# Performance work log

Hardware: AMD Instinct MI355X
Metric: run time of the kernel (lower is better)

The kernel has to match this reference:

```python
import jax, jax.numpy as jnp
import numpy as np

B, T, E, D, V, L, A = 32, 800, 512, 1024, 5000, 149, 512
SOS, EOS = 1, 2


def setup_inputs() -> dict:
    key = jax.random.key(0)
    ks = jax.random.split(key, 20)
    s = 0.02
    inp = {
        'hpad': jax.random.normal(ks[0], (B, T, E), dtype=jnp.float32),
        'hlen': jax.random.randint(ks[1], (B,), T // 2, T + 1),
        'ys': jax.random.randint(ks[2], (B, L), 3, V),
        # embedding + output projection
        'embed': jax.random.normal(ks[3], (V, D), dtype=jnp.float32) * s,
        'W_out': jax.random.normal(ks[4], (V, D), dtype=jnp.float32) * s,
        'b_out': jnp.zeros((V,), dtype=jnp.float32),
        # additive attention params
        'W_enc': jax.random.normal(ks[5], (E, A), dtype=jnp.float32) * s,
        'W_dec': jax.random.normal(ks[6], (D, A), dtype=jnp.float32) * s,
        'v_att': jax.random.normal(ks[7], (A,), dtype=jnp.float32) * s,
        # LSTMCell layer 0: input = [ey; att_c] of size D+E
        'W_ih0': jax.random.normal(ks[8], (4 * D, D + E), dtype=jnp.float32) * s,
        'b_ih0': jnp.zeros((4 * D,), dtype=jnp.float32),
        'W_hh0': jax.random.normal(ks[9], (4 * D, D), dtype=jnp.float32) * s,
        'b_hh0': jnp.zeros((4 * D,), dtype=jnp.float32),
        # LSTMCell layer 1: input = z0 of size D
        'W_ih1': jax.random.normal(ks[10], (4 * D, D), dtype=jnp.float32) * s,
        'b_ih1': jnp.zeros((4 * D,), dtype=jnp.float32),
        'W_hh1': jax.random.normal(ks[11], (4 * D, D), dtype=jnp.float32) * s,
        'b_hh1': jnp.zeros((4 * D,), dtype=jnp.float32),
    }
    return inp


def _lstm_cell(x, h, c, W_ih, b_ih, W_hh, b_hh):
    # torch.nn.LSTMCell gate order: i, f, g, o
    g = x @ W_ih.T + b_ih + h @ W_hh.T + b_hh
    i, f, gg, o = jnp.split(g, 4, axis=-1)
    c2 = jax.nn.sigmoid(f) * c + jax.nn.sigmoid(i) * jnp.tanh(gg)
    h2 = jax.nn.sigmoid(o) * jnp.tanh(c2)
    return h2, c2


def reference(hpad, hlen, ys, embed, W_out, b_out, W_enc, W_dec, v_att,
              W_ih0, b_ih0, W_hh0, b_hh0, W_ih1, b_ih1, W_hh1, b_hh1):
    mask = jnp.arange(T)[None, :] < hlen[:, None]          # [B,T]
    hpad = hpad * mask[..., None]                          # mask_by_length
    ys_in = jnp.concatenate([jnp.full((B, 1), SOS, ys.dtype), ys], axis=1)   # [B,L+1]
    ys_out = jnp.concatenate([ys, jnp.full((B, 1), EOS, ys.dtype)], axis=1)  # [B,L+1]
    eys = embed[ys_in]                                     # [B,L+1,D]
    pe = jnp.einsum('bte,ea->bta', hpad, W_enc)            # precomputed enc proj

    def step(carry, ey):
        z0, c0, z1, c1 = carry
        # additive attention: e = v^T tanh(W_enc h + W_dec z0)
        e = jnp.einsum('bta,a->bt', jnp.tanh(pe + (z0 @ W_dec)[:, None, :]), v_att)
        e = jnp.where(mask, e, -1e30)
        w = jax.nn.softmax(e, axis=-1)                     # [B,T]
        att_c = jnp.einsum('bt,bte->be', w, hpad)          # [B,E]
        z0, c0 = _lstm_cell(jnp.concatenate([ey, att_c], axis=1), z0, c0,
                            W_ih0, b_ih0, W_hh0, b_hh0)
        z1, c1 = _lstm_cell(z0, z1, c1, W_ih1, b_ih1, W_hh1, b_hh1)
        logits = z1 @ W_out.T + b_out                      # [B,V]
        return (z0, c0, z1, c1), logits

    z = jnp.zeros((B, D), dtype=hpad.dtype)
    carry0 = (z, z, z, z)
    _, logits = jax.lax.scan(step, carry0, eys.transpose(1, 0, 2))  # [L+1,B,V]
    logits = logits.transpose(1, 0, 2)                     # [B,L+1,V]

    logp = jax.nn.log_softmax(logits, axis=-1)
    nll = -jnp.take_along_axis(logp, ys_out[..., None], axis=-1)[..., 0]
    # F.cross_entropy mean, then * (mean(len ys_in) - 1) = * L
    loss = nll.mean() * L
    acc = (jnp.argmax(logits, axis=-1) == ys_out).mean()
    return loss, acc
```

## Files before the change

kernel.cpp:

```cpp
#include <hip/hip_runtime.h>


typedef unsigned short u16;
typedef unsigned char u8;
typedef unsigned int u32;
typedef long long i64;
typedef unsigned long long u64;
typedef float f32x4 __attribute__((ext_vector_type(4)));
typedef float f32x2 __attribute__((ext_vector_type(2)));
typedef short s16x8 __attribute__((ext_vector_type(8)));

constexpr int cB = 32, cT = 800, cE = 512, cD = 1024, cV = 5000, cL = 149,
              cNS = 150, cA = 512;
constexpr int SOS = 1, EOS = 2;
constexpr int NBLK = 256;
constexpr float DS = 1.0f / 128.0f;

constexpr int AFLAG = 0;
constexpr int Z0FLAG = 256;
constexpr int HH1FLAG = 384;
constexpr int Z1FLAG = 512;
constexpr int G0FLAG = 640;
constexpr int QFLAG = 704;
constexpr int SFLAG = 720;
constexpr int ZDONEW = 976;

__device__ __forceinline__ float bf2f(u16 x){
  union { u32 u; float f; } v; v.u = ((u32)x) << 16; return v.f;
}
__device__ __forceinline__ u16 f2bf(float f){
  union { float f; u32 u; } v; v.f = f;
  u32 r = v.u + 0x7FFFu + ((v.u >> 16) & 1u);
  return (u16)(r >> 16);
}
__device__ __forceinline__ float frcp(float x){ return __builtin_amdgcn_rcpf(x); }
__device__ __forceinline__ float fsigm(float x){ return frcp(1.f + __expf(-x)); }
__device__ __forceinline__ float ftanh(float x){
  float u = __expf(2.f * x);
  return 1.f - 2.f * frcp(u + 1.f);
}
__device__ __forceinline__ f32x4 MFMA(s16x8 a, s16x8 b, f32x4 c){
  return __builtin_amdgcn_mfma_f32_16x16x32_bf16(a, b, c, 0, 0, 0);
}
__device__ __forceinline__ f32x4 MFMA8(i64 a, i64 b, f32x4 c){
  return __builtin_amdgcn_mfma_f32_16x16x32_fp8_fp8(a, b, c, 0, 0, 0);
}
__device__ __forceinline__ s16x8 LD8(const u16* p){ return *(const s16x8*)p; }
__device__ __forceinline__ u8 f2fp8(float x){
  return (u8)(__builtin_amdgcn_cvt_pk_fp8_f32(x, x, 0, false) & 0xFF);
}
__device__ __forceinline__ u32 pk4(float a, float b, float c, float d){
  u32 w = (u32)__builtin_amdgcn_cvt_pk_fp8_f32(a, b, 0, false);
  w = (u32)__builtin_amdgcn_cvt_pk_fp8_f32(c, d, (int)w, true);
  return w;
}
__device__ __forceinline__ void unpack8(u32 lo, u32 hi, float* o){
  f32x2 a = __builtin_amdgcn_cvt_pk_f32_fp8((int)lo, false);
  f32x2 b = __builtin_amdgcn_cvt_pk_f32_fp8((int)lo, true);
  f32x2 c = __builtin_amdgcn_cvt_pk_f32_fp8((int)hi, false);
  f32x2 d = __builtin_amdgcn_cvt_pk_f32_fp8((int)hi, true);
  o[0]=a[0]; o[1]=a[1]; o[2]=b[0]; o[3]=b[1];
  o[4]=c[0]; o[5]=c[1]; o[6]=d[0]; o[7]=d[1];
}

__device__ __forceinline__ float ld_sc(const float* p){
  return __hip_atomic_load(p, __ATOMIC_RELAXED, __HIP_MEMORY_SCOPE_AGENT);
}
__device__ __forceinline__ void st_sc(float* p, float v){
  __hip_atomic_store(p, v, __ATOMIC_RELAXED, __HIP_MEMORY_SCOPE_AGENT);
}
__device__ __forceinline__ u64 ld_sc8(const void* p){
  return __hip_atomic_load((const u64*)p, __ATOMIC_RELAXED, __HIP_MEMORY_SCOPE_AGENT);
}
__device__ __forceinline__ u32 ld_su(const u32* p){
  return __hip_atomic_load(p, __ATOMIC_RELAXED, __HIP_MEMORY_SCOPE_AGENT);
}
__device__ __forceinline__ void st_su(u32* p, u32 v){
  __hip_atomic_store(p, v, __ATOMIC_RELAXED, __HIP_MEMORY_SCOPE_AGENT);
}
__device__ __forceinline__ void st_scb(u8* p, u8 v){
  __hip_atomic_store(p, v, __ATOMIC_RELAXED, __HIP_MEMORY_SCOPE_AGENT);
}

__device__ __forceinline__ void pollge(const u32* f, int n, u32 target){
  const int lane = threadIdx.x & 63;
  for(;;){
    bool ok = true;
    for (int i = lane; i < n; i += 64) ok &= (ld_su(f + i) >= target);
    if (__all(ok)) break;
    __builtin_amdgcn_s_sleep(1);
  }
}
__device__ __forceinline__ void sig(u32* f, u32 v){
  asm volatile("s_waitcnt vmcnt(0)" ::: "memory");
  st_su(f, v);
}

__global__ void k_init(u32* ctl, float* q, float* c0, float* c1, u8* z1f8,
                       float* att_acc, float* att_l){
  int i = blockIdx.x * blockDim.x + threadIdx.x, n = gridDim.x * blockDim.x;
  for (int k = i; k < 1024; k += n) ctl[k] = 0;
  for (int k = i; k < cB * cA; k += n) q[k] = 0.f;
  for (int k = i; k < 2 * cB * cD; k += n){ c0[k] = 0.f; c1[k] = 0.f; }
  for (int k = i; k < cB * cD / 4; k += n) ((u32*)z1f8)[k] = 0;
  for (int k = i; k < 2 * cB * cE; k += n) att_acc[k] = 0.f;
  for (int k = i; k < 2 * cB; k += n) att_l[k] = 0.f;
}

__global__ void k_cvt(const float* __restrict__ s, u16* __restrict__ d, int n4){
  int i = blockIdx.x * blockDim.x + threadIdx.x, st = gridDim.x * blockDim.x;
  for (int k = i; k < n4; k += st){
    float4 v = ((const float4*)s)[k];
    ushort4 o; o.x = f2bf(v.x); o.y = f2bf(v.y); o.z = f2bf(v.z); o.w = f2bf(v.w);
    ((ushort4*)d)[k] = o;
  }
}

__global__ void k_cvt8I(const float* __restrict__ s, u8* __restrict__ d, int n){
  int i = blockIdx.x * blockDim.x + threadIdx.x, st = gridDim.x * blockDim.x;
  for (int k = i; k < n; k += st){
    int row = k >> 6, grp = k & 63;
    const float4* p = (const float4*)(s + (size_t)row * 512 + grp * 8);
    float4 v0 = p[0], v1 = p[1];
    u32 lo = pk4(v0.x, v0.y, v0.z, v0.w);
    u32 hi = pk4(v1.x, v1.y, v1.z, v1.w);
    *(uint2*)(d + (size_t)row * 1024 + grp * 16 + 8) = make_uint2(lo, hi);
  }
}

__global__ void k_slice(const float* __restrict__ s, u16* __restrict__ d, int n,
                        int cshift, int srcld, int coff){
  int i = blockIdx.x * blockDim.x + threadIdx.x, st = gridDim.x * blockDim.x;
  int cmask = (1 << cshift) - 1;
  for (int k = i; k < n; k += st){
    int r = k >> cshift, c = k & cmask;
    d[k] = f2bf(s[(size_t)r * srcld + coff + c]);
  }
}

__global__ void k_transp(const float* __restrict__ s, u16* __restrict__ d, int n,
                         int rshift, int csrc){
  int i = blockIdx.x * blockDim.x + threadIdx.x, st = gridDim.x * blockDim.x;
  int mask = (1 << rshift) - 1;
  for (int k = i; k < n; k += st){
    int dd = k & mask, a = k >> rshift;
    d[k] = f2bf(s[(size_t)dd * csrc + a]);
  }
}

__global__ void k_bias(const float* a, const float* b, float* o, int n){
  int i = blockIdx.x * blockDim.x + threadIdx.x, st = gridDim.x * blockDim.x;
  for (int k = i; k < n; k += st) o[k] = a[k] + b[k];
}

__global__ void k_wf8perm(const float* __restrict__ s, u8* __restrict__ d,
                          int n4, int kshift, int srcld, int coff){
  int i = blockIdx.x * blockDim.x + threadIdx.x, st = gridDim.x * blockDim.x;
  int kmask = (1 << kshift) - 1;
  for (int k = i; k < n4; k += st){
    int flat = k * 4;
    int R = flat >> kshift, kk = flat & kmask;
    int j = R >> 5, jj = R & 31, g = jj >> 3, c = jj & 7;
    const float* p = s + (size_t)(g * 1024 + j * 8 + c) * srcld + coff + kk;
    ((u32*)d)[k] = pk4(p[0]*16.f, p[1]*16.f, p[2]*16.f, p[3]*16.f);
  }
}

__global__ void k_wf8(const float* __restrict__ s, u8* __restrict__ d, int n4){
  int i = blockIdx.x * blockDim.x + threadIdx.x, st = gridDim.x * blockDim.x;
  for (int k = i; k < n4; k += st){
    float4 v = ((const float4*)s)[k];
    ((u32*)d)[k] = pk4(v.x*16.f, v.y*16.f, v.z*16.f, v.w*16.f);
  }
}

__global__ void k_wf8t(const float* __restrict__ s, u8* __restrict__ d, int n4){
  int i = blockIdx.x * blockDim.x + threadIdx.x, st = gridDim.x * blockDim.x;
  for (int k = i; k < n4; k += st){
    int flat = k * 4;
    int a = flat >> 10, dd = flat & 1023;
    ((u32*)d)[k] = pk4(s[(size_t)(dd+0)*512 + a]*16.f,
                       s[(size_t)(dd+1)*512 + a]*16.f,
                       s[(size_t)(dd+2)*512 + a]*16.f,
                       s[(size_t)(dd+3)*512 + a]*16.f);
  }
}

__global__ void k_gather(const u16* __restrict__ embb, const int* __restrict__ ys,
                         u16* __restrict__ ey, int n16){
  int i = blockIdx.x * blockDim.x + threadIdx.x, st = gridDim.x * blockDim.x;
  for (int k = i; k < n16; k += st){
    int r = k >> 7, seg = k & 127;
    int s = r >> 5, b = r & 31;
    int tok = (s == 0) ? SOS : ys[b * cL + (s - 1)];
    ((uint4*)ey)[(size_t)r * 128 + seg] =
        ((const uint4*)embb)[(size_t)tok * 128 + seg];
  }
}

__global__ __launch_bounds__(512, 1) void k_pe2(const u16* __restrict__ A,
    const u16* __restrict__ Bw, u8* __restrict__ ph8){
  int tid = threadIdx.x, w = tid >> 6, l = tid & 63;
  int col = l & 15, kin = 8 * (l >> 4);
  int mw = w >> 2, nw = w & 3;
  int m0 = blockIdx.x * 128 + mw * 64;
  int n0 = nw * 128;
  f32x4 acc[4][8] = {};
  for (int kc = 0; kc < 16; ++kc){
    int k = kc * 32 + kin;
    s16x8 af[4], bf[8];
    #pragma unroll
    for (int i = 0; i < 4; ++i) af[i] = LD8(A + (size_t)(m0 + i*16 + col)*512 + k);
    #pragma unroll
    for (int j = 0; j < 8; ++j) bf[j] = LD8(Bw + (size_t)(n0 + j*16 + col)*512 + k);
    #pragma unroll
    for (int i = 0; i < 4; ++i)
      #pragma unroll
      for (int j = 0; j < 8; ++j) acc[i][j] = MFMA(af[i], bf[j], acc[i][j]);
  }
  int hi4 = (l >> 4) * 4;
  #pragma unroll
  for (int i = 0; i < 4; ++i)
    #pragma unroll
    for (int j = 0; j < 8; ++j){
      int a0 = n0 + j * 16 + col;
      size_t boff = ((size_t)(a0 >> 3) << 4) + (a0 & 7);
      #pragma unroll
      for (int r = 0; r < 4; ++r){
        int row = m0 + i * 16 + hi4 + r;
        ph8[(size_t)row * 1024 + boff] = f2fp8(acc[i][j][r]);
      }
    }
}

__global__ __launch_bounds__(512, 1) void k_ey2(const u16* __restrict__ ey,
    const u16* __restrict__ Wm, const float* __restrict__ bih0,
    const float* __restrict__ bhh0, u16* __restrict__ eyproj,
    float* __restrict__ g0buf){
  int tid = threadIdx.x, w = tid >> 6, l = tid & 63;
  int col = l & 15, kin = 8 * (l >> 4);
  int mw = w >> 2, nw = w & 3;
  int m0 = blockIdx.x * 128 + mw * 64;
  int n0 = blockIdx.y * 512 + nw * 128;
  f32x4 acc[4][8] = {};
  for (int kc = 0; kc < 32; ++kc){
    int k = kc * 32 + kin;
    s16x8 af[4], bf[8];
    #pragma unroll
    for (int i = 0; i < 4; ++i){
      int ar = m0 + i * 16 + col; ar = (ar < 4800) ? ar : 0;
      af[i] = LD8(ey + (size_t)ar * 1024 + k);
    }
    #pragma unroll
    for (int j = 0; j < 8; ++j) bf[j] = LD8(Wm + (size_t)(n0 + j*16 + col)*1024 + k);
    #pragma unroll
    for (int i = 0; i < 4; ++i)
      #pragma unroll
      for (int j = 0; j < 8; ++j) acc[i][j] = MFMA(af[i], bf[j], acc[i][j]);
  }
  int hi4 = (l >> 4) * 4;
  #pragma unroll
  for (int i = 0; i < 4; ++i)
    #pragma unroll
    for (int j = 0; j < 8; ++j){
      int jc = n0 + j * 16 + col;
      float bj = bih0[jc] + bhh0[jc];
      #pragma unroll
      for (int r = 0; r < 4; ++r){
        int row = m0 + i * 16 + hi4 + r;
        if (row < 4800){
          float val = acc[i][j][r] + bj;
          eyproj[(size_t)row * 4096 + jc] = f2bf(val);
          if (row < 32) g0buf[(size_t)row * 4096 + jc] = val;
        }
      }
    }
}

struct LoopArgs {
  const int* hlen;
  const u8* ph8;
  const u16* eyproj;
  const u8* Wapf8; const u8* Whh1f8; const u8* Wih1f8; const u8* Whh0f8;
  const u8* WdecTf8;
  const float* vatt; const float* bias01;
  float* q; float* att_acc; float* att_l;
  float* g0buf; float* hh1buf; u8* z0f8; u8* z1f8;
  float* c0; float* c1; u16* z1all;
  u32* ctl;
};

constexpr int SPZ = 1048;
constexpr int SPA = 536;

struct P1Lds { float red[8][512]; float ls[8]; };
struct GvLds { u8 x[32 * SPZ]; float acc[8][2][16][17]; };
union LoopLds { P1Lds p1; GvLds gv; };

__device__ __forceinline__ void stage_att(LoopLds& L, const float* att_acc,
                                          const float* att_l, int tid){
  int r = tid >> 4, c0 = (tid & 15) * 32;
  float sc = 8.0f * frcp(ld_sc(att_l + r));
  const float* src = att_acc + r * 512 + c0;
  u32 wd[8];
  #pragma unroll
  for (int i = 0; i < 8; ++i){
    union { u64 q; float f[2]; } a, b;
    a.q = ld_sc8(src + i * 4);
    b.q = ld_sc8(src + i * 4 + 2);
    wd[i] = pk4(a.f[0] * sc, a.f[1] * sc, b.f[0] * sc, b.f[1] * sc);
  }
  uint2* dst = (uint2*)&L.gv.x[r * SPA + c0];
  dst[0] = make_uint2(wd[0], wd[1]);
  dst[1] = make_uint2(wd[2], wd[3]);
  dst[2] = make_uint2(wd[4], wd[5]);
  dst[3] = make_uint2(wd[6], wd[7]);
}

__device__ __forceinline__ void stage_z(LoopLds& L, const u8* zf8, int tid){
  int r = tid >> 4, c0 = (tid & 15) * 64;
  const u8* src = zf8 + (size_t)r * 1024 + c0;
  u64 v[8];
  #pragma unroll
  for (int i = 0; i < 8; ++i) v[i] = ld_sc8(src + i * 8);
  u64* dst = (u64*)&L.gv.x[r * SPZ + c0];
  #pragma unroll
  for (int i = 0; i < 8; ++i) dst[i] = v[i];
}

template<int KH, int ITERS, int SP>
__device__ __forceinline__ void gemv_reg(const i64* wreg, LoopLds& L, int tid){
  const int w = tid >> 6, l = tid & 63;
  const int col = l & 15, kin = 8 * (l >> 4);
  const int kh = (KH == 4) ? (w & 3) : (w & 1);
  constexpr int KB = ITERS * 32;
  const u8* xr = &L.gv.x[col * SP + kh * KB + kin];
  f32x4 a0 = {0.f,0.f,0.f,0.f}, a1 = {0.f,0.f,0.f,0.f};
  #pragma unroll
  for (int kc = 0; kc < ITERS; ++kc){
    i64 x0 = *(const i64*)(xr + kc * 32);
    i64 x1 = *(const i64*)(xr + 16 * SP + kc * 32);
    a0 = MFMA8(x0, wreg[kc], a0);
    a1 = MFMA8(x1, wreg[kc], a1);
  }
  const int hi4 = (l >> 4) * 4;
  #pragma unroll
  for (int r = 0; r < 4; ++r){
    L.gv.acc[w][0][hi4 + r][col] = a0[r];
    L.gv.acc[w][1][hi4 + r][col] = a1[r];
  }
}

__global__ __launch_bounds__(512, 1) void k_loop(LoopArgs g_){
  __shared__ __align__(16) LoopLds L;
  __shared__ __align__(16) u8 ph8_lds[100 * 1024];
  const int blk = blockIdx.x, tid = threadIdx.x;
  const int w = tid >> 6, l = tid & 63;
  const int col = l & 15, kin = 8 * (l >> 4);
  const int b_att = blk >> 3, oct = blk & 7;
  const int hl = g_.hlen[b_att];
  const int t0 = oct * 100;
  const int t1 = (t0 + 100 < hl) ? t0 + 100 : hl;
  const int nrow = t1 - t0;
  u32* ctl = g_.ctl;
  float vv[8];
  #pragma unroll
  for (int i = 0; i < 8; ++i) vv[i] = g_.vatt[l * 8 + i];
  for (int idx = tid; idx < nrow * 64; idx += 512){
    int rr = idx >> 6, gg = idx & 63;
    *(uint4*)&ph8_lds[rr * 1024 + gg * 16] =
        *(const uint4*)(g_.ph8 + ((size_t)b_att * cT + t0 + rr) * 1024 + gg * 16);
  }
  i64 wB[8], wC[16];
  {
    const int nt4 = w >> 2, kh4 = w & 3;
    const int nt2 = w >> 1, kh2 = w & 1;
    if (blk < 128){
      const u8* wr = g_.Wapf8 + (size_t)blk * 32 * 512 +
                     (size_t)(nt4 * 16 + col) * 512 + kh4 * 128 + kin;
      #pragma unroll
      for (int kc = 0; kc < 4; ++kc) wB[kc] = *(const i64*)(wr + kc * 32);
      const u8* wr2 = g_.Wih1f8 + (size_t)blk * 32 * 1024 +
                      (size_t)(nt4 * 16 + col) * 1024 + kh4 * 256 + kin;
      #pragma unroll
      for (int kc = 0; kc < 8; ++kc) wC[kc] = *(const i64*)(wr2 + kc * 32);
    } else {
      const u8* wr = g_.Whh1f8 + (size_t)(blk - 128) * 32 * 1024 +
                     (size_t)(nt4 * 16 + col) * 1024 + kh4 * 256 + kin;
      #pragma unroll
      for (int kc = 0; kc < 8; ++kc) wB[kc] = *(const i64*)(wr + kc * 32);
      if (blk < 192){
        const u8* wr2 = g_.Whh0f8 + (size_t)(blk - 128) * 64 * 1024 +
                        (size_t)(nt2 * 16 + col) * 1024 + kh2 * 512 + kin;
        #pragma unroll
        for (int kc = 0; kc < 16; ++kc) wC[kc] = *(const i64*)(wr2 + kc * 32);
      } else if (blk < 208){
        const u8* wr2 = g_.WdecTf8 + (size_t)(blk - 192) * 32 * 1024 +
                        (size_t)(nt4 * 16 + col) * 1024 + kh4 * 256 + kin;
        #pragma unroll
        for (int kc = 0; kc < 8; ++kc) wC[kc] = *(const i64*)(wr2 + kc * 32);
      }
    }
  }
  __syncthreads();

  for (int s = 0; s < cNS; ++s){
    const int p = s & 1;
    if (nrow > 0){
      if (tid < 64){
        pollge(ctl + QFLAG, 16, (u32)s);
        if (tid == 0){
          u32 need = (u32)(s >> 1);
          while (ld_su(&ctl[ZDONEW + p * 16]) < need)
            __builtin_amdgcn_s_sleep(1);
        }
      }
      __syncthreads();
      float qv[8];
      const float* qb = g_.q + b_att * cA + l * 8;
      #pragma unroll
      for (int i = 0; i < 8; ++i) qv[i] = ld_sc(qb + i);
      float acc8[8] = {0.f,0.f,0.f,0.f,0.f,0.f,0.f,0.f};
      float lsum = 0.f;
      for (int t = t0 + w; t < t1; t += 8){
        uint4 v = *(const uint4*)&ph8_lds[(t - t0) * 1024 + l * 16];
        float x[8]; unpack8(v.x, v.y, x);
        float e_ = 0.f;
        #pragma unroll
        for (int i = 0; i < 8; ++i) e_ += vv[i] * ftanh(x[i] + qv[i]);
        #pragma unroll
        for (int m = 1; m < 64; m <<= 1) e_ += __shfl_xor(e_, m, 64);
        float wt = __expf(e_);
        lsum += wt;
        float h[8]; unpack8(v.z, v.w, h);
        #pragma unroll
        for (int i = 0; i < 8; ++i) acc8[i] = fmaf(wt, h[i], acc8[i]);
      }
      *(f32x4*)&L.p1.red[w][l * 8]     = *(f32x4*)&acc8[0];
      *(f32x4*)&L.p1.red[w][l * 8 + 4] = *(f32x4*)&acc8[4];
      if (l == 0) L.p1.ls[w] = lsum;
      __syncthreads();
      float vsum = 0.f;
      #pragma unroll
      for (int ww = 0; ww < 8; ++ww) vsum += L.p1.red[ww][tid];
      atomicAdd(&g_.att_acc[((size_t)p * cB + b_att) * cE + tid], vsum);
      if (tid == 0){
        float ls = 0.f;
        #pragma unroll
        for (int i = 0; i < 8; ++i) ls += L.p1.ls[i];
        atomicAdd(&g_.att_l[p * cB + b_att], ls);
      }
    }
    __syncthreads();
    if (tid == 0) sig(&ctl[AFLAG + blk], (u32)(s + 1));
    if (blk < 128){
      if (tid < 64){
        pollge(ctl + AFLAG, 256, (u32)(s + 1));
        pollge(ctl + G0FLAG, 64, (u32)s);
      }
      __syncthreads();
      stage_att(L, g_.att_acc + (size_t)p * cB * cE, g_.att_l + p * cB, tid);
      __syncthreads();
      if (tid == 0) sig(&ctl[SFLAG + p * 128 + blk], (u32)(s >> 1) + 1u);
      float gpre[4], cpre = 0.f;
      int bb = tid >> 3, dc = tid & 7, d = blk * 8 + dc;
      if (tid < 256){
        #pragma unroll
        for (int g = 0; g < 4; ++g)
          gpre[g] = ld_sc(&g_.g0buf[(size_t)p * cB * 4096 + bb * 4096 + g * 1024 + d]);
        cpre = g_.c0[(size_t)p * cB * cD + bb * cD + d];
      }
      gemv_reg<4, 4, SPA>(wB, L, tid);
      __syncthreads();
      if (tid < 256){
        int mt = bb >> 4, rr = bb & 15;
        float gate[4];
        #pragma unroll
        for (int g = 0; g < 4; ++g){
          int jj = g * 8 + dc;
          float v = 0.f;
          #pragma unroll
          for (int kh = 0; kh < 4; ++kh)
            v += L.gv.acc[(jj >> 4) * 4 + kh][mt][rr][jj & 15];
          gate[g] = v * DS + gpre[g];
        }
        float c = fsigm(gate[1]) * cpre + fsigm(gate[0]) * ftanh(gate[2]);
        float z = fsigm(gate[3]) * ftanh(c);
        g_.c0[(size_t)(p ^ 1) * cB * cD + bb * cD + d] = c;
        st_scb(&g_.z0f8[bb * cD + d], f2fp8(z * 8.f));
      }
      __syncthreads();
      if (tid == 0) sig(&ctl[Z0FLAG + blk], (u32)(s + 1));
    } else {
      if (tid < 64) pollge(ctl + Z1FLAG, 128, (u32)s);
      __syncthreads();
      stage_z(L, g_.z1f8, tid);
      __syncthreads();
      gemv_reg<4, 8, SPZ>(wB, L, tid);
      __syncthreads();
      {
        const int jb = (blk - 128) * 32;
        int bb = tid >> 4, j2 = (tid & 15) * 2;
        int mt = bb >> 4, rr = bb & 15;
        #pragma unroll
        for (int k = 0; k < 2; ++k){
          int jj = j2 + k;
          float v = 0.f;
          #pragma unroll
          for (int kh = 0; kh < 4; ++kh)
            v += L.gv.acc[(jj >> 4) * 4 + kh][mt][rr][jj & 15];
          st_sc(&g_.hh1buf[bb * 4096 + jb + jj], v * DS + g_.bias01[jb + jj]);
        }
      }
      __syncthreads();
      if (tid == 0) sig(&ctl[HH1FLAG + (blk - 128)], (u32)(s + 1));
    }
    if (blk < 128){
      if (tid < 64){
        pollge(ctl + Z0FLAG, 128, (u32)(s + 1));
        pollge(ctl + HH1FLAG, 128, (u32)(s + 1));
      }
      __syncthreads();
      stage_z(L, g_.z0f8, tid);
      __syncthreads();
      float hpre[4], cpre = 0.f;
      int bb = tid >> 3, dc = tid & 7, d = blk * 8 + dc;
      if (tid < 256){
        #pragma unroll
        for (int g = 0; g < 4; ++g)
          hpre[g] = ld_sc(&g_.hh1buf[bb * 4096 + g * 1024 + d]);
        cpre = g_.c1[(size_t)p * cB * cD + bb * cD + d];
      }
      gemv_reg<4, 8, SPZ>(wC, L, tid);
      __syncthreads();
      if (tid < 256){
        int mt = bb >> 4, rr = bb & 15;
        float gate[4];
        #pragma unroll
        for (int g = 0; g < 4; ++g){
          int jj = g * 8 + dc;
          float v = 0.f;
          #pragma unroll
          for (int kh = 0; kh < 4; ++kh)
            v += L.gv.acc[(jj >> 4) * 4 + kh][mt][rr][jj & 15];
          gate[g] = v * DS + hpre[g];
        }
        float c = fsigm(gate[1]) * cpre + fsigm(gate[0]) * ftanh(gate[2]);
        float z = fsigm(gate[3]) * ftanh(c);
        g_.c1[(size_t)(p ^ 1) * cB * cD + bb * cD + d] = c;
        g_.z1all[((size_t)s + 1) * cB * cD + bb * cD + d] = f2bf(z);
        st_scb(&g_.z1f8[bb * cD + d], f2fp8(z * 8.f));
      }
      __syncthreads();
      if (tid == 0) sig(&ctl[Z1FLAG + blk], (u32)(s + 1));
    } else if (blk < 192){
      if (tid < 64) pollge(ctl + Z0FLAG, 128, (u32)(s + 1));
      __syncthreads();
      stage_z(L, g_.z0f8, tid);
      __syncthreads();
      gemv_reg<2, 16, SPZ>(wC, L, tid);
      __syncthreads();
      if (s < cNS - 1){
        const int jb = (blk - 128) * 64;
        int bb = tid >> 4, j4 = (tid & 15) * 4;
        int mt = bb >> 4, rr = bb & 15;
        const u16* eyr = g_.eyproj + (((size_t)(s + 1) * cB + bb) * 4096) + jb + j4;
        #pragma unroll
        for (int k = 0; k < 4; ++k){
          int jj = j4 + k;
          float v = 0.f;
          #pragma unroll
          for (int kh = 0; kh < 2; ++kh)
            v += L.gv.acc[(jj >> 4) * 2 + kh][mt][rr][jj & 15];
          st_sc(&g_.g0buf[(size_t)(p ^ 1) * cB * 4096 + bb * 4096 + jb + jj],
                v * DS + bf2f(eyr[k]));
        }
      }
      __syncthreads();
      if (tid == 0) sig(&ctl[G0FLAG + (blk - 128)], (u32)(s + 1));
    } else if (blk < 208){
      if (tid < 64) pollge(ctl + Z0FLAG, 128, (u32)(s + 1));
      __syncthreads();
      stage_z(L, g_.z0f8, tid);
      __syncthreads();
      gemv_reg<4, 8, SPZ>(wC, L, tid);
      __syncthreads();
      if (s < cNS - 1){
        const int jb = (blk - 192) * 32;
        int bb = tid >> 4, j2 = (tid & 15) * 2;
        int mt = bb >> 4, rr = bb & 15;
        #pragma unroll
        for (int k = 0; k < 2; ++k){
          int jj = j2 + k;
          float v = 0.f;
          #pragma unroll
          for (int kh = 0; kh < 4; ++kh)
            v += L.gv.acc[(jj >> 4) * 4 + kh][mt][rr][jj & 15];
          st_sc(&g_.q[bb * cA + jb + jj], v * DS);
        }
      }
      __syncthreads();
      if (tid == 0) sig(&ctl[QFLAG + (blk - 192)], (u32)(s + 1));
    } else if (blk == 208){
      if (tid < 64) pollge(ctl + SFLAG + p * 128, 128, (u32)(s >> 1) + 1u);
      __syncthreads();
      {
        float* aa = g_.att_acc + (size_t)p * cB * cE;
        for (int i = tid; i < cB * cE; i += 512) st_sc(&aa[i], 0.f);
        if (tid < cB) st_sc(&g_.att_l[p * cB + tid], 0.f);
      }
      __syncthreads();
      if (tid == 0) sig(&ctl[ZDONEW + p * 16], (u32)(s >> 1) + 1u);
    }
  }
}

__global__ __launch_bounds__(256) void k_ce1(const u16* __restrict__ z1all,
    const u16* __restrict__ Woutb, const float* __restrict__ bout,
    const int* __restrict__ ys, float* __restrict__ pmax, float* __restrict__ psum,
    int* __restrict__ pai, float* __restrict__ tgtl){
  int blk = blockIdx.x;
  int sc = blk / 40, vc = blk % 40;
  int tid = threadIdx.x, w = tid >> 6, l = tid & 63;
  int kin = 8 * (l >> 4), col = l & 15;
  int v0 = vc * 128 + w * 32;
  int vA = v0 + col, vB = v0 + 16 + col;
  float boA = (vA < cV) ? bout[vA] : 0.f;
  float boB = (vB < cV) ? bout[vB] : 0.f;
  const u16* wrA = Woutb + (size_t)((vA < cV) ? vA : cV - 1) * cD;
  const u16* wrB = Woutb + (size_t)((vB < cV) ? vB : cV - 1) * cD;
  __shared__ int tgt_sh[32];
  __shared__ float rsm[4][32], rss[4][32];
  __shared__ int rsi[4][32];
  for (int si = 0; si < 5; ++si){
    int s = sc * 5 + si;
    if (tid < 32) tgt_sh[tid] = (s < cL) ? ys[tid * cL + s] : EOS;
    __syncthreads();
    const u16* z1s = z1all + ((size_t)s + 1) * cB * cD;
    f32x4 aA0 = {0.f,0.f,0.f,0.f}, aA1 = {0.f,0.f,0.f,0.f};
    f32x4 aB0 = {0.f,0.f,0.f,0.f}, aB1 = {0.f,0.f,0.f,0.f};
    for (int kc = 0; kc < 32; ++kc){
      int k = kc * 32 + kin;
      s16x8 x0 = LD8(z1s + (size_t)col * cD + k);
      s16x8 x1 = LD8(z1s + (size_t)(16 + col) * cD + k);
      s16x8 bA = LD8(wrA + k);
      s16x8 bB = LD8(wrB + k);
      aA0 = MFMA(x0, bA, aA0); aA1 = MFMA(x1, bA, aA1);
      aB0 = MFMA(x0, bB, aB0); aB1 = MFMA(x1, bB, aB1);
    }
    #pragma unroll
    for (int mt = 0; mt < 2; ++mt)
    #pragma unroll
    for (int reg = 0; reg < 4; ++reg){
      int row = mt * 16 + (l >> 4) * 4 + reg;
      float va = (mt ? aA1[reg] : aA0[reg]) + boA; if (vA >= cV) va = -1e30f;
      float vb = (mt ? aB1[reg] : aB0[reg]) + boB; if (vB >= cV) vb = -1e30f;
      int tg = tgt_sh[row];
      if (vA == tg) tgtl[(size_t)s * cB + row] = va;
      if (vB == tg) tgtl[(size_t)s * cB + row] = vb;
      float mx = fmaxf(va, vb);
      int ix = (va >= vb) ? vA : vB;
      #pragma unroll
      for (int m = 1; m < 16; m <<= 1){
        float om = __shfl_xor(mx, m, 64);
        int oi = __shfl_xor(ix, m, 64);
        if (om > mx || (om == mx && oi < ix)){ mx = om; ix = oi; }
      }
      float se = __expf(va - mx) + __expf(vb - mx);
      #pragma unroll
      for (int m = 1; m < 16; m <<= 1) se += __shfl_xor(se, m, 64);
      if ((l & 15) == 0){ rsm[w][row] = mx; rss[w][row] = se; rsi[w][row] = ix; }
    }
    __syncthreads();
    if (tid < 32){
      int b = tid;
      float gm = -1e30f;
      #pragma unroll
      for (int w2 = 0; w2 < 4; ++w2) gm = fmaxf(gm, rsm[w2][b]);
      float gs = 0.f; float bv = -1e30f; int bix = 0x7fffffff;
      #pragma unroll
      for (int w2 = 0; w2 < 4; ++w2){
        gs += rss[w2][b] * __expf(rsm[w2][b] - gm);
        float v = rsm[w2][b]; int ii = rsi[w2][b];
        if (v > bv || (v == bv && ii < bix)){ bv = v; bix = ii; }
      }
      size_t o = ((size_t)s * cB + b) * 40 + vc;
      pmax[o] = gm; psum[o] = gs; pai[o] = bix;
    }
    __syncthreads();
  }
}

__global__ __launch_bounds__(64) void k_ce2(const float* __restrict__ pmax,
    const float* __restrict__ psum, const int* __restrict__ pai,
    const float* __restrict__ tgtl, const int* __restrict__ ys,
    float* __restrict__ cestep){
  int s = blockIdx.x, tid = threadIdx.x;
  float nll = 0.f, cor = 0.f;
  if (tid < 32){
    int b = tid;
    size_t o = ((size_t)s * cB + b) * 40;
    float gm = -1e30f;
    for (int c = 0; c < 40; ++c) gm = fmaxf(gm, pmax[o + c]);
    float gs = 0.f; float bv = -1e30f; int bix = 0x7fffffff;
    for (int c = 0; c < 40; ++c){
      gs += psum[o + c] * __expf(pmax[o + c] - gm);
      float v = pmax[o + c]; int ii = pai[o + c];
      if (v > bv || (v == bv && ii < bix)){ bv = v; bix = ii; }
    }
    nll = __logf(gs) + gm - tgtl[(size_t)s * cB + b];
    int tgt = (s < cL) ? ys[b * cL + s] : EOS;
    cor = (bix == tgt) ? 1.f : 0.f;
  }
  #pragma unroll
  for (int m = 1; m < 64; m <<= 1){
    nll += __shfl_xor(nll, m, 64); cor += __shfl_xor(cor, m, 64);
  }
  if (tid == 0){ cestep[s * 2] = nll; cestep[s * 2 + 1] = cor; }
}

__global__ __launch_bounds__(256) void k_ce3(const float* __restrict__ cestep,
                                             float* __restrict__ out){
  int tid = threadIdx.x;
  float nll = 0.f, cor = 0.f;
  for (int s = tid; s < cNS; s += 256){ nll += cestep[s * 2]; cor += cestep[s * 2 + 1]; }
  __shared__ float sn[4], sc_[4];
  int w = tid >> 6, l = tid & 63;
  #pragma unroll
  for (int m = 1; m < 64; m <<= 1){
    nll += __shfl_xor(nll, m, 64); cor += __shfl_xor(cor, m, 64);
  }
  if (l == 0){ sn[w] = nll; sc_[w] = cor; }
  __syncthreads();
  if (tid == 0){
    float a = sn[0] + sn[1] + sn[2] + sn[3];
    float b = sc_[0] + sc_[1] + sc_[2] + sc_[3];
    out[0] = a / (float)(cB * cNS) * (float)cL;
    out[1] = b / (float)(cB * cNS);
  }
}

extern "C" void kernel_launch(void* const* d_in, const int* in_sizes, int n_in,
                              void* d_out, int out_size, void* d_ws, size_t ws_size,
                              hipStream_t stream){
  const float* hpad = (const float*)d_in[0];
  const int*   hlen = (const int*)d_in[1];
  const int*   ys   = (const int*)d_in[2];
  const float* embed= (const float*)d_in[3];
  const float* Wout = (const float*)d_in[4];
  const float* bout = (const float*)d_in[5];
  const float* Wenc = (const float*)d_in[6];
  const float* Wdec = (const float*)d_in[7];
  const float* vatt = (const float*)d_in[8];
  const float* Wih0 = (const float*)d_in[9];
  const float* bih0 = (const float*)d_in[10];
  const float* Whh0 = (const float*)d_in[11];
  const float* bhh0 = (const float*)d_in[12];
  const float* Wih1 = (const float*)d_in[13];
  const float* bih1 = (const float*)d_in[14];
  const float* Whh1 = (const float*)d_in[15];
  const float* bhh1 = (const float*)d_in[16];
  (void)in_sizes; (void)n_in; (void)out_size; (void)ws_size;

  char* base = (char*)d_ws;
  size_t off = 0;
  auto alloc = [&](size_t bytes) -> void* {
    void* r = base + off; off += (bytes + 255) & ~(size_t)255; return r;
  };
  u32*   ctl     = (u32*)  alloc(1024 * 4);
  u16*   hpadM   = (u16*)  alloc((size_t)cB * cT * cE * 2);
  u8*    ph8     = (u8*)   alloc((size_t)cB * cT * 1024);
  u16*   embb    = (u16*)  alloc((size_t)cV * cD * 2);
  u16*   ey      = (u16*)  alloc((size_t)cNS * cB * cD * 2);
  u16*   eyproj  = (u16*)  alloc((size_t)cNS * cB * 4096 * 2);
  u16*   z1all   = (u16*)  alloc((size_t)(cNS + 1) * cB * cD * 2);
  u16*   WencT   = (u16*)  alloc((size_t)cA * cE * 2);
  u16*   Wih0m   = (u16*)  alloc((size_t)4096 * cD * 2);
  u16*   Woutb   = (u16*)  alloc((size_t)cV * cD * 2);
  u8*    Wapf8   = (u8*)   alloc((size_t)4096 * 512);
  u8*    Wih1f8  = (u8*)   alloc((size_t)4096 * 1024);
  u8*    Whh1f8  = (u8*)   alloc((size_t)4096 * 1024);
  u8*    Whh0f8  = (u8*)   alloc((size_t)4096 * 1024);
  u8*    WdecTf8 = (u8*)   alloc((size_t)512 * 1024);
  float* bias01  = (float*)alloc(4096 * 4);
  float* qbuf    = (float*)alloc((size_t)cB * cA * 4);
  float* att_acc = (float*)alloc((size_t)2 * cB * cE * 4);
  float* att_l   = (float*)alloc((size_t)2 * cB * 4);
  float* g0buf   = (float*)alloc((size_t)2 * cB * 4096 * 4);
  float* hh1buf  = (float*)alloc((size_t)cB * 4096 * 4);
  u8*    z0f8    = (u8*)   alloc((size_t)cB * cD);
  u8*    z1f8    = (u8*)   alloc((size_t)cB * cD);
  float* c0      = (float*)alloc((size_t)2 * cB * cD * 4);
  float* c1      = (float*)alloc((size_t)2 * cB * cD * 4);
  float* pmax    = (float*)alloc((size_t)cNS * cB * 40 * 4);
  float* psum    = (float*)alloc((size_t)cNS * cB * 40 * 4);
  int*   pai     = (int*)  alloc((size_t)cNS * cB * 40 * 4);
  float* tgtl    = (float*)alloc((size_t)cNS * cB * 4);
  float* cestep  = (float*)alloc((size_t)cNS * 2 * 4);

  k_init<<<64, 256, 0, stream>>>(ctl, qbuf, c0, c1, z1f8, att_acc, att_l);
  k_cvt<<<2048, 256, 0, stream>>>(hpad, hpadM, cB * cT * cE / 4);
  k_cvt8I<<<1024, 256, 0, stream>>>(hpad, ph8, cB * cT * 64);
  k_cvt<<<2048, 256, 0, stream>>>(embed, embb, cV * cD / 4);
  k_cvt<<<2048, 256, 0, stream>>>(Wout, Woutb, cV * cD / 4);
  k_slice<<<1024, 256, 0, stream>>>(Wih0, Wih0m, 4096 * cD, 10, 1536, 0);
  k_transp<<<256, 256, 0, stream>>>(Wenc, WencT, cA * cE, 9, cA);
  k_bias<<<16, 256, 0, stream>>>(bih1, bhh1, bias01, 4096);
  k_wf8perm<<<512, 256, 0, stream>>>(Wih0, Wapf8, 4096 * 512 / 4, 9, 1536, 1024);
  k_wf8perm<<<1024, 256, 0, stream>>>(Wih1, Wih1f8, 4096 * 1024 / 4, 10, 1024, 0);
  k_wf8<<<1024, 256, 0, stream>>>(Whh1, Whh1f8, 4096 * 1024 / 4);
  k_wf8<<<1024, 256, 0, stream>>>(Whh0, Whh0f8, 4096 * 1024 / 4);
  k_wf8t<<<128, 256, 0, stream>>>(Wdec, WdecTf8, 512 * 1024 / 4);
  k_gather<<<1200, 256, 0, stream>>>(embb, ys, ey, cNS * cB * 128);
  k_pe2<<<200, 512, 0, stream>>>(hpadM, WencT, ph8);
  k_ey2<<<dim3(38, 8), 512, 0, stream>>>(ey, Wih0m, bih0, bhh0, eyproj, g0buf);

  LoopArgs la;
  la.hlen = hlen; la.ph8 = ph8; la.eyproj = eyproj;
  la.Wapf8 = Wapf8; la.Whh1f8 = Whh1f8; la.Wih1f8 = Wih1f8;
  la.Whh0f8 = Whh0f8; la.WdecTf8 = WdecTf8;
  la.vatt = vatt; la.bias01 = bias01;
  la.q = qbuf; la.att_acc = att_acc; la.att_l = att_l;
  la.g0buf = g0buf; la.hh1buf = hh1buf; la.z0f8 = z0f8; la.z1f8 = z1f8;
  la.c0 = c0; la.c1 = c1; la.z1all = z1all; la.ctl = ctl;
  k_loop<<<NBLK, 512, 0, stream>>>(la);

  k_ce1<<<1200, 256, 0, stream>>>(z1all, Woutb, bout, ys, pmax, psum, pai, tgtl);
  k_ce2<<<cNS, 64, 0, stream>>>(pmax, psum, pai, tgtl, ys, cestep);
  k_ce3<<<1, 256, 0, stream>>>(cestep, (float*)d_out);
}
```

Measured before the change: 4.852 ms.

## Replace per-buffer flag barriers with step-tagged bf16 data words in persistent loop

Intermediate buffers exchanged between blocks of the persistent decoder loop (q, hh1, g0) now hold bf16 values with the step number in the upper 16 bits. Consumers poll the data words directly instead of waiting on separate per-producer flag arrays, which removes several barrier/signal round trips per step. The attention accumulator also moves from fp32 atomicAdd to packed bf16 atomic adds. This cuts synchronisation latency and atomic traffic, at the cost of bf16 precision in the gate pre-activations and attention accumulation, and it relies on each tagged word being stored atomically.

```diff
diff --git a/kernel.cpp b/kernel.cpp
--- a/kernel.cpp
+++ b/kernel.cpp
@@ -18,12 +18,9 @@
 
 constexpr int AFLAG = 0;
 constexpr int Z0FLAG = 256;
-constexpr int HH1FLAG = 384;
-constexpr int Z1FLAG = 512;
-constexpr int G0FLAG = 640;
-constexpr int QFLAG = 704;
-constexpr int SFLAG = 720;
-constexpr int ZDONEW = 976;
+constexpr int Z1FLAG = 384;
+constexpr int SFLAG = 512;
+constexpr int ZDONE = 768;
 
 __device__ __forceinline__ float bf2f(u16 x){
   union { u32 u; float f; } v; v.u = ((u32)x) << 16; return v.f;
@@ -72,6 +69,9 @@
 __device__ __forceinline__ u64 ld_sc8(const void* p){
   return __hip_atomic_load((const u64*)p, __ATOMIC_RELAXED, __HIP_MEMORY_SCOPE_AGENT);
 }
+__device__ __forceinline__ void st_sc8(void* p, u64 v){
+  __hip_atomic_store((u64*)p, v, __ATOMIC_RELAXED, __HIP_MEMORY_SCOPE_AGENT);
+}
 __device__ __forceinline__ u32 ld_su(const u32* p){
   return __hip_atomic_load(p, __ATOMIC_RELAXED, __HIP_MEMORY_SCOPE_AGENT);
 }
@@ -80,6 +80,10 @@
 }
 __device__ __forceinline__ void st_scb(u8* p, u8 v){
   __hip_atomic_store(p, v, __ATOMIC_RELAXED, __HIP_MEMORY_SCOPE_AGENT);
+}
+__device__ __forceinline__ void atomic_pk_bf16(u32* dst, u32 data){
+  asm volatile("global_atomic_pk_add_bf16 %0, %1, off"
+               :: "v"(dst), "v"(data) : "memory");
 }
 
 __device__ __forceinline__ void pollge(const u32* f, int n, u32 target){
@@ -96,15 +100,16 @@
   st_su(f, v);
 }
 
-__global__ void k_init(u32* ctl, float* q, float* c0, float* c1, u8* z1f8,
-                       float* att_acc, float* att_l){
+__global__ void k_init(u32* ctl, u32* qt, float* c0, float* c1, u8* z1f8,
+                       u32* att_pk, float* att_l, u32* hh1t){
   int i = blockIdx.x * blockDim.x + threadIdx.x, n = gridDim.x * blockDim.x;
   for (int k = i; k < 1024; k += n) ctl[k] = 0;
-  for (int k = i; k < cB * cA; k += n) q[k] = 0.f;
+  for (int k = i; k < cB * cA; k += n) qt[k] = 0;
   for (int k = i; k < 2 * cB * cD; k += n){ c0[k] = 0.f; c1[k] = 0.f; }
   for (int k = i; k < cB * cD / 4; k += n) ((u32*)z1f8)[k] = 0;
-  for (int k = i; k < 2 * cB * cE; k += n) att_acc[k] = 0.f;
+  for (int k = i; k < 2 * cB * 256; k += n) att_pk[k] = 0;
   for (int k = i; k < 2 * cB; k += n) att_l[k] = 0.f;
+  for (int k = i; k < cB * 4096; k += n) hh1t[k] = 0xFFFF0000u;
 }
 
 __global__ void k_cvt(const float* __restrict__ s, u16* __restrict__ d, int n4){
@@ -236,7 +241,7 @@
 __global__ __launch_bounds__(512, 1) void k_ey2(const u16* __restrict__ ey,
     const u16* __restrict__ Wm, const float* __restrict__ bih0,
     const float* __restrict__ bhh0, u16* __restrict__ eyproj,
-    float* __restrict__ g0buf){
+    u32* __restrict__ g0t){
   int tid = threadIdx.x, w = tid >> 6, l = tid & 63;
   int col = l & 15, kin = 8 * (l >> 4);
   int mw = w >> 2, nw = w & 3;
@@ -271,7 +276,7 @@
         if (row < 4800){
           float val = acc[i][j][r] + bj;
           eyproj[(size_t)row * 4096 + jc] = f2bf(val);
-          if (row < 32) g0buf[(size_t)row * 4096 + jc] = val;
+          if (row < 32) g0t[(size_t)row * 4096 + jc] = (u32)f2bf(val);
         }
       }
     }
@@ -284,8 +289,8 @@
   const u8* Wapf8; const u8* Whh1f8; const u8* Wih1f8; const u8* Whh0f8;
   const u8* WdecTf8;
   const float* vatt; const float* bias01;
-  float* q; float* att_acc; float* att_l;
-  float* g0buf; float* hh1buf; u8* z0f8; u8* z1f8;
+  u32* qt; u32* att_pk; float* att_l;
+  u32* g0t; u32* hh1t; u8* z0f8; u8* z1f8;
   float* c0; float* c1; u16* z1all;
   u32* ctl;
 };
@@ -293,24 +298,26 @@
 constexpr int SPZ = 1048;
 constexpr int SPA = 536;
 
-struct P1Lds { float red[8][512]; float ls[8]; };
+struct P1Lds { float red[8][512]; float ls[8]; float qsh[512]; };
 struct GvLds { u8 x[32 * SPZ]; float acc[8][2][16][17]; };
 union LoopLds { P1Lds p1; GvLds gv; };
 
-__device__ __forceinline__ void stage_att(LoopLds& L, const float* att_acc,
+__device__ __forceinline__ void stage_att(LoopLds& L, const u32* att_pk,
                                           const float* att_l, int tid){
-  int r = tid >> 4, c0 = (tid & 15) * 32;
+  int r = tid >> 4, cp = (tid & 15) * 16;
   float sc = 8.0f * frcp(ld_sc(att_l + r));
-  const float* src = att_acc + r * 512 + c0;
+  const u32* src = att_pk + (size_t)r * 256 + cp;
+  u64 v[8];
+  #pragma unroll
+  for (int i = 0; i < 8; ++i) v[i] = ld_sc8(src + i * 2);
   u32 wd[8];
   #pragma unroll
   for (int i = 0; i < 8; ++i){
-    union { u64 q; float f[2]; } a, b;
-    a.q = ld_sc8(src + i * 4);
-    b.q = ld_sc8(src + i * 4 + 2);
-    wd[i] = pk4(a.f[0] * sc, a.f[1] * sc, b.f[0] * sc, b.f[1] * sc);
-  }
-  uint2* dst = (uint2*)&L.gv.x[r * SPA + c0];
+    u32 a = (u32)v[i], b = (u32)(v[i] >> 32);
+    wd[i] = pk4(bf2f((u16)a) * sc, bf2f((u16)(a >> 16)) * sc,
+                bf2f((u16)b) * sc, bf2f((u16)(b >> 16)) * sc);
+  }
+  uint2* dst = (uint2*)&L.gv.x[r * SPA + (tid & 15) * 32];
   dst[0] = make_uint2(wd[0], wd[1]);
   dst[1] = make_uint2(wd[2], wd[3]);
   dst[2] = make_uint2(wd[4], wd[5]);
@@ -407,19 +414,33 @@
   for (int s = 0; s < cNS; ++s){
     const int p = s & 1;
     if (nrow > 0){
-      if (tid < 64){
-        pollge(ctl + QFLAG, 16, (u32)s);
-        if (tid == 0){
-          u32 need = (u32)(s >> 1);
-          while (ld_su(&ctl[ZDONEW + p * 16]) < need)
-            __builtin_amdgcn_s_sleep(1);
+      if (w == 0){
+        const u32* qrow = g_.qt + b_att * cA + l * 8;
+        const u64 tmask = 0xFFFF0000FFFF0000ULL;
+        const u64 texp = ((u64)(u32)s << 48) | ((u64)(u32)s << 16);
+        u64 qw[4];
+        for(;;){
+          bool ok = true;
+          #pragma unroll
+          for (int i = 0; i < 4; ++i){
+            qw[i] = ld_sc8(qrow + i * 2);
+            ok &= ((qw[i] & tmask) == texp);
+          }
+          if (l == 0)
+            ok &= (ld_su(&ctl[ZDONE + p * 16]) >= (u32)(s >> 1));
+          if (__all(ok)) break;
+          __builtin_amdgcn_s_sleep(1);
+        }
+        #pragma unroll
+        for (int i = 0; i < 4; ++i){
+          L.p1.qsh[l * 8 + 2*i]     = bf2f((u16)(qw[i] & 0xFFFF));
+          L.p1.qsh[l * 8 + 2*i + 1] = bf2f((u16)((qw[i] >> 32) & 0xFFFF));
         }
       }
       __syncthreads();
       float qv[8];
-      const float* qb = g_.q + b_att * cA + l * 8;
-      #pragma unroll
-      for (int i = 0; i < 8; ++i) qv[i] = ld_sc(qb + i);
+      #pragma unroll
+      for (int i = 0; i < 8; ++i) qv[i] = L.p1.qsh[l * 8 + i];
       float acc8[8] = {0.f,0.f,0.f,0.f,0.f,0.f,0.f,0.f};
       float lsum = 0.f;
       for (int t = t0 + w; t < t1; t += 8){
@@ -440,10 +461,16 @@
       *(f32x4*)&L.p1.red[w][l * 8 + 4] = *(f32x4*)&acc8[4];
       if (l == 0) L.p1.ls[w] = lsum;
       __syncthreads();
-      float vsum = 0.f;
-      #pragma unroll
-      for (int ww = 0; ww < 8; ++ww) vsum += L.p1.red[ww][tid];
-      atomicAdd(&g_.att_acc[((size_t)p * cB + b_att) * cE + tid], vsum);
+      if (tid < 256){
+        float v0 = 0.f, v1 = 0.f;
+        #pragma unroll
+        for (int ww = 0; ww < 8; ++ww){
+          v0 += L.p1.red[ww][tid * 2];
+          v1 += L.p1.red[ww][tid * 2 + 1];
+        }
+        u32 pk = ((u32)f2bf(v1) << 16) | (u32)f2bf(v0);
+        atomic_pk_bf16(g_.att_pk + ((size_t)p * cB + b_att) * 256 + tid, pk);
+      }
       if (tid == 0){
         float ls = 0.f;
         #pragma unroll
@@ -454,25 +481,33 @@
     __syncthreads();
     if (tid == 0) sig(&ctl[AFLAG + blk], (u32)(s + 1));
     if (blk < 128){
-      if (tid < 64){
-        pollge(ctl + AFLAG, 256, (u32)(s + 1));
-        pollge(ctl + G0FLAG, 64, (u32)s);
-      }
-      __syncthreads();
-      stage_att(L, g_.att_acc + (size_t)p * cB * cE, g_.att_l + p * cB, tid);
+      if (tid < 64) pollge(ctl + AFLAG, 256, (u32)(s + 1));
+      __syncthreads();
+      stage_att(L, g_.att_pk + (size_t)p * cB * 256, g_.att_l + p * cB, tid);
       __syncthreads();
       if (tid == 0) sig(&ctl[SFLAG + p * 128 + blk], (u32)(s >> 1) + 1u);
-      float gpre[4], cpre = 0.f;
+      u32 gw[4]; bool gok = true; float cpre = 0.f;
       int bb = tid >> 3, dc = tid & 7, d = blk * 8 + dc;
       if (tid < 256){
         #pragma unroll
-        for (int g = 0; g < 4; ++g)
-          gpre[g] = ld_sc(&g_.g0buf[(size_t)p * cB * 4096 + bb * 4096 + g * 1024 + d]);
+        for (int g = 0; g < 4; ++g){
+          gw[g] = ld_su(&g_.g0t[(size_t)bb * 4096 + g * 1024 + d]);
+          gok &= ((gw[g] >> 16) == (u32)s);
+        }
         cpre = g_.c0[(size_t)p * cB * cD + bb * cD + d];
       }
       gemv_reg<4, 4, SPA>(wB, L, tid);
       __syncthreads();
       if (tid < 256){
+        while (!__all(gok)){
+          gok = true;
+          #pragma unroll
+          for (int g = 0; g < 4; ++g){
+            gw[g] = ld_su(&g_.g0t[(size_t)bb * 4096 + g * 1024 + d]);
+            gok &= ((gw[g] >> 16) == (u32)s);
+          }
+          if (!__all(gok)) __builtin_amdgcn_s_sleep(1);
+        }
         int mt = bb >> 4, rr = bb & 15;
         float gate[4];
         #pragma unroll
@@ -482,7 +517,7 @@
           #pragma unroll
           for (int kh = 0; kh < 4; ++kh)
             v += L.gv.acc[(jj >> 4) * 4 + kh][mt][rr][jj & 15];
-          gate[g] = v * DS + gpre[g];
+          gate[g] = v * DS + bf2f((u16)(gw[g] & 0xFFFF));
         }
         float c = fsigm(gate[1]) * cpre + fsigm(gate[0]) * ftanh(gate[2]);
         float z = fsigm(gate[3]) * ftanh(c);
@@ -502,6 +537,7 @@
         const int jb = (blk - 128) * 32;
         int bb = tid >> 4, j2 = (tid & 15) * 2;
         int mt = bb >> 4, rr = bb & 15;
+        u32 ow[2];
         #pragma unroll
         for (int k = 0; k < 2; ++k){
           int jj = j2 + k;
@@ -509,31 +545,38 @@
           #pragma unroll
           for (int kh = 0; kh < 4; ++kh)
             v += L.gv.acc[(jj >> 4) * 4 + kh][mt][rr][jj & 15];
-          st_sc(&g_.hh1buf[bb * 4096 + jb + jj], v * DS + g_.bias01[jb + jj]);
-        }
-      }
-      __syncthreads();
-      if (tid == 0) sig(&ctl[HH1FLAG + (blk - 128)], (u32)(s + 1));
+          ow[k] = ((u32)(s + 1) << 16) | (u32)f2bf(v * DS + g_.bias01[jb + jj]);
+        }
+        st_sc8(&g_.hh1t[(size_t)bb * 4096 + jb + j2], ((u64)ow[1] << 32) | ow[0]);
+      }
     }
     if (blk < 128){
-      if (tid < 64){
-        pollge(ctl + Z0FLAG, 128, (u32)(s + 1));
-        pollge(ctl + HH1FLAG, 128, (u32)(s + 1));
-      }
+      if (tid < 64) pollge(ctl + Z0FLAG, 128, (u32)(s + 1));
       __syncthreads();
       stage_z(L, g_.z0f8, tid);
       __syncthreads();
-      float hpre[4], cpre = 0.f;
+      u32 hw[4]; bool hok = true; float cpre = 0.f;
       int bb = tid >> 3, dc = tid & 7, d = blk * 8 + dc;
       if (tid < 256){
         #pragma unroll
-        for (int g = 0; g < 4; ++g)
-          hpre[g] = ld_sc(&g_.hh1buf[bb * 4096 + g * 1024 + d]);
+        for (int g = 0; g < 4; ++g){
+          hw[g] = ld_su(&g_.hh1t[(size_t)bb * 4096 + g * 1024 + d]);
+          hok &= ((hw[g] >> 16) == (u32)(s + 1));
+        }
         cpre = g_.c1[(size_t)p * cB * cD + bb * cD + d];
       }
       gemv_reg<4, 8, SPZ>(wC, L, tid);
       __syncthreads();
       if (tid < 256){
+        while (!__all(hok)){
+          hok = true;
+          #pragma unroll
+          for (int g = 0; g < 4; ++g){
+            hw[g] = ld_su(&g_.hh1t[(size_t)bb * 4096 + g * 1024 + d]);
+            hok &= ((hw[g] >> 16) == (u32)(s + 1));
+          }
+          if (!__all(hok)) __builtin_amdgcn_s_sleep(1);
+        }
         int mt = bb >> 4, rr = bb & 15;
         float gate[4];
         #pragma unroll
@@ -543,7 +586,7 @@
           #pragma unroll
           for (int kh = 0; kh < 4; ++kh)
             v += L.gv.acc[(jj >> 4) * 4 + kh][mt][rr][jj & 15];
-          gate[g] = v * DS + hpre[g];
+          gate[g] = v * DS + bf2f((u16)(hw[g] & 0xFFFF));
         }
         float c = fsigm(gate[1]) * cpre + fsigm(gate[0]) * ftanh(gate[2]);
         float z = fsigm(gate[3]) * ftanh(c);
@@ -565,6 +608,7 @@
         int bb = tid >> 4, j4 = (tid & 15) * 4;
         int mt = bb >> 4, rr = bb & 15;
         const u16* eyr = g_.eyproj + (((size_t)(s + 1) * cB + bb) * 4096) + jb + j4;
+        u32 ow[4];
         #pragma unroll
         for (int k = 0; k < 4; ++k){
           int jj = j4 + k;
@@ -572,12 +616,11 @@
           #pragma unroll
           for (int kh = 0; kh < 2; ++kh)
             v += L.gv.acc[(jj >> 4) * 2 + kh][mt][rr][jj & 15];
-          st_sc(&g_.g0buf[(size_t)(p ^ 1) * cB * 4096 + bb * 4096 + jb + jj],
-                v * DS + bf2f(eyr[k]));
-        }
-      }
-      __syncthreads();
-      if (tid == 0) sig(&ctl[G0FLAG + (blk - 128)], (u32)(s + 1));
+          ow[k] = ((u32)(s + 1) << 16) | (u32)f2bf(v * DS + bf2f(eyr[k]));
+        }
+        st_sc8(&g_.g0t[(size_t)bb * 4096 + jb + j4],     ((u64)ow[1] << 32) | ow[0]);
+        st_sc8(&g_.g0t[(size_t)bb * 4096 + jb + j4 + 2], ((u64)ow[3] << 32) | ow[2]);
+      }
     } else if (blk < 208){
       if (tid < 64) pollge(ctl + Z0FLAG, 128, (u32)(s + 1));
       __syncthreads();
@@ -589,6 +632,7 @@
         const int jb = (blk - 192) * 32;
         int bb = tid >> 4, j2 = (tid & 15) * 2;
         int mt = bb >> 4, rr = bb & 15;
+        u32 ow[2];
         #pragma unroll
         for (int k = 0; k < 2; ++k){
           int jj = j2 + k;
@@ -596,21 +640,20 @@
           #pragma unroll
           for (int kh = 0; kh < 4; ++kh)
             v += L.gv.acc[(jj >> 4) * 4 + kh][mt][rr][jj & 15];
-          st_sc(&g_.q[bb * cA + jb + jj], v * DS);
-        }
-      }
-      __syncthreads();
-      if (tid == 0) sig(&ctl[QFLAG + (blk - 192)], (u32)(s + 1));
+          ow[k] = ((u32)(s + 1) << 16) | (u32)f2bf(v * DS);
+        }
+        st_sc8(&g_.qt[(size_t)bb * cA + jb + j2], ((u64)ow[1] << 32) | ow[0]);
+      }
     } else if (blk == 208){
       if (tid < 64) pollge(ctl + SFLAG + p * 128, 128, (u32)(s >> 1) + 1u);
       __syncthreads();
       {
-        float* aa = g_.att_acc + (size_t)p * cB * cE;
-        for (int i = tid; i < cB * cE; i += 512) st_sc(&aa[i], 0.f);
+        u32* aa = g_.att_pk + (size_t)p * cB * 256;
+        for (int i = tid; i < cB * 256; i += 512) st_su(&aa[i], 0);
         if (tid < cB) st_sc(&g_.att_l[p * cB + tid], 0.f);
       }
       __syncthreads();
-      if (tid == 0) sig(&ctl[ZDONEW + p * 16], (u32)(s >> 1) + 1u);
+      if (tid == 0) sig(&ctl[ZDONE + p * 16], (u32)(s >> 1) + 1u);
     }
   }
 }
@@ -783,11 +826,11 @@
   u8*    Whh0f8  = (u8*)   alloc((size_t)4096 * 1024);
   u8*    WdecTf8 = (u8*)   alloc((size_t)512 * 1024);
   float* bias01  = (float*)alloc(4096 * 4);
-  float* qbuf    = (float*)alloc((size_t)cB * cA * 4);
-  float* att_acc = (float*)alloc((size_t)2 * cB * cE * 4);
+  u32*   qt      = (u32*)  alloc((size_t)cB * cA * 4);
+  u32*   att_pk  = (u32*)  alloc((size_t)2 * cB * 256 * 4);
   float* att_l   = (float*)alloc((size_t)2 * cB * 4);
-  float* g0buf   = (float*)alloc((size_t)2 * cB * 4096 * 4);
-  float* hh1buf  = (float*)alloc((size_t)cB * 4096 * 4);
+  u32*   g0t     = (u32*)  alloc((size_t)cB * 4096 * 4);
+  u32*   hh1t    = (u32*)  alloc((size_t)cB * 4096 * 4);
   u8*    z0f8    = (u8*)   alloc((size_t)cB * cD);
   u8*    z1f8    = (u8*)   alloc((size_t)cB * cD);
   float* c0      = (float*)alloc((size_t)2 * cB * cD * 4);
@@ -798,7 +841,7 @@
   float* tgtl    = (float*)alloc((size_t)cNS * cB * 4);
   float* cestep  = (float*)alloc((size_t)cNS * 2 * 4);
 
-  k_init<<<64, 256, 0, stream>>>(ctl, qbuf, c0, c1, z1f8, att_acc, att_l);
+  k_init<<<64, 256, 0, stream>>>(ctl, qt, c0, c1, z1f8, att_pk, att_l, hh1t);
   k_cvt<<<2048, 256, 0, stream>>>(hpad, hpadM, cB * cT * cE / 4);
   k_cvt8I<<<1024, 256, 0, stream>>>(hpad, ph8, cB * cT * 64);
   k_cvt<<<2048, 256, 0, stream>>>(embed, embb, cV * cD / 4);
@@ -813,15 +856,15 @@
   k_wf8t<<<128, 256, 0, stream>>>(Wdec, WdecTf8, 512 * 1024 / 4);
   k_gather<<<1200, 256, 0, stream>>>(embb, ys, ey, cNS * cB * 128);
   k_pe2<<<200, 512, 0, stream>>>(hpadM, WencT, ph8);
-  k_ey2<<<dim3(38, 8), 512, 0, stream>>>(ey, Wih0m, bih0, bhh0, eyproj, g0buf);
+  k_ey2<<<dim3(38, 8), 512, 0, stream>>>(ey, Wih0m, bih0, bhh0, eyproj, g0t);
 
   LoopArgs la;
   la.hlen = hlen; la.ph8 = ph8; la.eyproj = eyproj;
   la.Wapf8 = Wapf8; la.Whh1f8 = Whh1f8; la.Wih1f8 = Wih1f8;
   la.Whh0f8 = Whh0f8; la.WdecTf8 = WdecTf8;
   la.vatt = vatt; la.bias01 = bias01;
-  la.q = qbuf; la.att_acc = att_acc; la.att_l = att_l;
-  la.g0buf = g0buf; la.hh1buf = hh1buf; la.z0f8 = z0f8; la.z1f8 = z1f8;
+  la.qt = qt; la.att_pk = att_pk; la.att_l = att_l;
+  la.g0t = g0t; la.hh1t = hh1t; la.z0f8 = z0f8; la.z1f8 = z1f8;
   la.c0 = c0; la.c1 = c1; la.z1all = z1all; la.ctl = ctl;
   k_loop<<<NBLK, 512, 0, stream>>>(la);
 
```

Result: faster. 4.028 ms, median of 2 (-17.0%).
